# Optimization experiments

Hardware: AMD Instinct MI355X
Metric: run time of the kernel (lower is better)

Reference implementation:

```python
import jax, jax.numpy as jnp
import numpy as np

N_NODES = 150000
D = 64
N_EDGES = 2000000  # bidirectional: 2 * num_train_edges


def setup_inputs() -> dict:
    key = jax.random.key(0)
    k1, k2, k3, k4, k5 = jax.random.split(key, 5)
    nodes_emb = jax.random.normal(k1, (N_NODES, D), dtype=jnp.float32)
    src = jax.random.randint(k2, (N_EDGES,), 0, N_NODES, dtype=jnp.int64 if jax.config.jax_enable_x64 else jnp.int32).astype(jnp.int32)
    dst = jax.random.randint(k3, (N_EDGES,), 0, N_NODES, dtype=jnp.int32)
    W1 = jax.random.normal(k4, (2 * D, D), dtype=jnp.float32) * (1.0 / np.sqrt(2 * D))
    b1 = jnp.zeros((D,), dtype=jnp.float32)
    W2 = jax.random.normal(k5, (D, 1), dtype=jnp.float32) * (1.0 / np.sqrt(D))
    b2 = jnp.zeros((1,), dtype=jnp.float32)
    return {"nodes_emb": nodes_emb, "src": src, "dst": dst,
            "W1": W1, "b1": b1, "W2": W2, "b2": b2}


def reference(nodes_emb, src, dst, W1, b1, W2, b2):
    # Gather per-edge endpoint embeddings and concat: [E, 2D]
    emb_src = nodes_emb[src]          # [E, D]
    emb_dst = nodes_emb[dst]          # [E, D]
    edge_emb = jnp.concatenate([emb_src, emb_dst], axis=1)  # [E, 2D]
    # 2-layer MLP edge scorer: Linear(2D->D) -> ReLU -> Linear(D->1)
    h = jax.nn.relu(edge_emb @ W1 + b1)  # [E, D]
    edge_logits = h @ W2 + b2            # [E, 1]
    return edge_logits
```

## Files before the change

### kernel.cpp

```cpp
#include <hip/hip_runtime.h>

typedef __attribute__((ext_vector_type(8))) short bf16x8;
typedef __attribute__((ext_vector_type(4))) float f32x4;
typedef __attribute__((ext_vector_type(4))) unsigned int u32x4;

#define LDSTR 136
#define TPW 8

static __device__ __forceinline__ unsigned int pack2bf(float x, float y) {
  unsigned int ux = __builtin_bit_cast(unsigned int, x);
  ux += 0x7fffu + ((ux >> 16) & 1u);
  unsigned int uy = __builtin_bit_cast(unsigned int, y);
  uy += 0x7fffu + ((uy >> 16) & 1u);
  return (ux >> 16) | (uy & 0xffff0000u);
}
static __device__ __forceinline__ unsigned short f2bf_s(float x) {
  unsigned int ux = __builtin_bit_cast(unsigned int, x);
  ux += 0x7fffu + ((ux >> 16) & 1u);
  return (unsigned short)(ux >> 16);
}
static __device__ __forceinline__ bf16x8 make_afrag(float4 lo, float4 hi) {
  u32x4 p;
  p[0] = pack2bf(lo.x, lo.y);
  p[1] = pack2bf(lo.z, lo.w);
  p[2] = pack2bf(hi.x, hi.y);
  p[3] = pack2bf(hi.z, hi.w);
  return __builtin_bit_cast(bf16x8, p);
}

__global__ __launch_bounds__(256) void node_proj(
    const float* __restrict__ emb,
    const float* __restrict__ W1,
    unsigned short* __restrict__ P,
    unsigned short* __restrict__ Q,
    int N)
{
  __shared__ unsigned short ls_w1t[64 * LDSTR];
  const int tid  = threadIdx.x;
  const int wave = tid >> 6;
  const int lane = tid & 63;
  const int l15  = lane & 15;
  const int quad = lane >> 4;

  for (int i = tid; i < 64 * 128; i += 256) {
    int n = i >> 7, k = i & 127;
    ls_w1t[n * LDSTR + k] = f2bf_s(W1[k * 64 + n]);
  }
  __syncthreads();

  bf16x8 bfragP[4][2], bfragQ[4][2];
  #pragma unroll
  for (int tn = 0; tn < 4; ++tn)
    #pragma unroll
    for (int s = 0; s < 2; ++s) {
      bfragP[tn][s] = *(const bf16x8*)&ls_w1t[(tn * 16 + l15) * LDSTR + s * 32 + quad * 8];
      bfragQ[tn][s] = *(const bf16x8*)&ls_w1t[(tn * 16 + l15) * LDSTR + 64 + s * 32 + quad * 8];
    }

  const int tile = blockIdx.x * 4 + wave;
  const int base = tile * 16;
  if (base >= N) return;

  bf16x8 afr[2];
  {
    int node = base + l15;
    node = (node < N) ? node : N - 1;
    const float* rp = emb + (long long)node * 64 + quad * 8;
    afr[0] = make_afrag(*(const float4*)(rp),      *(const float4*)(rp + 4));
    afr[1] = make_afrag(*(const float4*)(rp + 32), *(const float4*)(rp + 36));
  }

  f32x4 aP[4], aQ[4];
  #pragma unroll
  for (int tn = 0; tn < 4; ++tn) { aP[tn] = (f32x4){0,0,0,0}; aQ[tn] = (f32x4){0,0,0,0}; }
  #pragma unroll
  for (int s = 0; s < 2; ++s)
    #pragma unroll
    for (int tn = 0; tn < 4; ++tn) {
      aP[tn] = __builtin_amdgcn_mfma_f32_16x16x32_bf16(afr[s], bfragP[tn][s], aP[tn], 0, 0, 0);
      aQ[tn] = __builtin_amdgcn_mfma_f32_16x16x32_bf16(afr[s], bfragQ[tn][s], aQ[tn], 0, 0, 0);
    }

  #pragma unroll
  for (int r = 0; r < 4; ++r) {
    const int m = base + quad * 4 + r;
    if (m < N) {
      #pragma unroll
      for (int tn = 0; tn < 4; ++tn) {
        P[(long long)m * 64 + tn * 16 + l15] = f2bf_s(aP[tn][r]);
        Q[(long long)m * 64 + tn * 16 + l15] = f2bf_s(aQ[tn][r]);
      }
    }
  }
}

__global__ __launch_bounds__(256) void edge_score(
    const unsigned short* __restrict__ P,
    const unsigned short* __restrict__ Q,
    const int*   __restrict__ src,
    const int*   __restrict__ dst,
    const float* __restrict__ b1,
    const float* __restrict__ W2,
    const float* __restrict__ b2,
    float*       __restrict__ out,
    int E)
{
  const int tid  = blockIdx.x * 256 + threadIdx.x;
  const int lane = threadIdx.x & 63;
  const int s    = lane & 7;
  const int g    = lane >> 3;
  const int wid  = tid >> 6;
  const int nwav = gridDim.x * 4;

  float b1v[8], w2v[8];
  {
    const float4 ba = *(const float4*)(b1 + s * 8);
    const float4 bb = *(const float4*)(b1 + s * 8 + 4);
    const float4 wa = *(const float4*)(W2 + s * 8);
    const float4 wb = *(const float4*)(W2 + s * 8 + 4);
    b1v[0]=ba.x; b1v[1]=ba.y; b1v[2]=ba.z; b1v[3]=ba.w;
    b1v[4]=bb.x; b1v[5]=bb.y; b1v[6]=bb.z; b1v[7]=bb.w;
    w2v[0]=wa.x; w2v[1]=wa.y; w2v[2]=wa.z; w2v[3]=wa.w;
    w2v[4]=wb.x; w2v[5]=wb.y; w2v[6]=wb.z; w2v[7]=wb.w;
  }
  const float b2v = b2[0];
  const int so16 = s * 8;

#define DOT8(PV, QV, ACC)                                                     \
  {                                                                           \
    u32x4 pu = __builtin_bit_cast(u32x4, PV);                                 \
    u32x4 qu = __builtin_bit_cast(u32x4, QV);                                 \
    _Pragma("unroll")                                                         \
    for (int i = 0; i < 4; ++i) {                                             \
      float pl = __builtin_bit_cast(float, pu[i] << 16);                      \
      float ph = __builtin_bit_cast(float, pu[i] & 0xffff0000u);              \
      float ql = __builtin_bit_cast(float, qu[i] << 16);                      \
      float qh = __builtin_bit_cast(float, qu[i] & 0xffff0000u);              \
      float h0 = fmaxf(pl + ql + b1v[2 * i], 0.f);                            \
      float h1 = fmaxf(ph + qh + b1v[2 * i + 1], 0.f);                        \
      ACC = __builtin_fmaf(h0, w2v[2 * i], ACC);                              \
      ACC = __builtin_fmaf(h1, w2v[2 * i + 1], ACC);                          \
    }                                                                         \
  }

  const int step = nwav * 16;
  for (int e0 = wid * 16; e0 < E; e0 += step) {
    int eA = e0 + g;
    int eB = e0 + 8 + g;
    const int eAc = (eA < E) ? eA : (E - 1);
    const int eBc = (eB < E) ? eB : (E - 1);
    const int siA = src[eAc], diA = dst[eAc];
    const int siB = src[eBc], diB = dst[eBc];

    const bf16x8 pvA = *(const bf16x8*)(P + (long long)siA * 64 + so16);
    const bf16x8 qvA = *(const bf16x8*)(Q + (long long)diA * 64 + so16);
    const bf16x8 pvB = *(const bf16x8*)(P + (long long)siB * 64 + so16);
    const bf16x8 qvB = *(const bf16x8*)(Q + (long long)diB * 64 + so16);

    float accA = 0.f, accB = 0.f;
    DOT8(pvA, qvA, accA);
    DOT8(pvB, qvB, accB);

    accA += __shfl_xor(accA, 1); accB += __shfl_xor(accB, 1);
    accA += __shfl_xor(accA, 2); accB += __shfl_xor(accB, 2);
    accA += __shfl_xor(accA, 4); accB += __shfl_xor(accB, 4);

    if (s == 0) {
      if (eA < E) out[eA] = accA + b2v;
      if (eB < E) out[eB] = accB + b2v;
    }
  }
#undef DOT8
}

__global__ __launch_bounds__(256) void edge_mlp_f32(
    const float* __restrict__ nodes_emb, const int* __restrict__ src,
    const int* __restrict__ dst, const float* __restrict__ W1,
    const float* __restrict__ b1, const float* __restrict__ W2,
    const float* __restrict__ b2, float* __restrict__ out, int E)
{
  __shared__ unsigned short ls_w1t[64 * LDSTR];
  __shared__ float ls_b1[64];
  __shared__ float ls_w2[64];
  const int tid = threadIdx.x, wave = tid >> 6, lane = tid & 63;
  const int l15 = lane & 15, quad = lane >> 4;
  for (int i = tid; i < 64 * 128; i += 256) {
    int n = i >> 7, k = i & 127;
    ls_w1t[n * LDSTR + k] = f2bf_s(W1[k * 64 + n]);
  }
  if (tid < 64) { ls_b1[tid] = b1[tid]; ls_w2[tid] = W2[tid]; }
  __syncthreads();
  bf16x8 bfrag[4][4];
  #pragma unroll
  for (int tn = 0; tn < 4; ++tn)
    #pragma unroll
    for (int s = 0; s < 4; ++s)
      bfrag[tn][s] = *(const bf16x8*)&ls_w1t[(tn * 16 + l15) * LDSTR + s * 32 + quad * 8];
  float myb1[4], myw2[4];
  #pragma unroll
  for (int tn = 0; tn < 4; ++tn) { myb1[tn] = ls_b1[tn*16+l15]; myw2[tn] = ls_w2[tn*16+l15]; }
  const float b2v = b2[0];
  const int wave_base = blockIdx.x * (TPW * 64) + wave * (TPW * 16);
  #pragma unroll 1
  for (int t = 0; t < TPW; ++t) {
    const int tile_base = wave_base + t * 16;
    if (tile_base >= E) break;
    const int e = tile_base + l15;
    const int si = src[e], di = dst[e];
    const float* srow = nodes_emb + (long long)si * 64 + quad * 8;
    const float* drow = nodes_emb + (long long)di * 64 + quad * 8;
    float4 v0 = *(const float4*)(srow),      v1 = *(const float4*)(srow + 4);
    float4 v2 = *(const float4*)(srow + 32), v3 = *(const float4*)(srow + 36);
    float4 v4 = *(const float4*)(drow),      v5 = *(const float4*)(drow + 4);
    float4 v6 = *(const float4*)(drow + 32), v7 = *(const float4*)(drow + 36);
    bf16x8 afr[4] = {make_afrag(v0,v1), make_afrag(v2,v3), make_afrag(v4,v5), make_afrag(v6,v7)};
    f32x4 acc[4];
    #pragma unroll
    for (int tn = 0; tn < 4; ++tn) acc[tn] = (f32x4){0.f,0.f,0.f,0.f};
    #pragma unroll
    for (int s = 0; s < 4; ++s)
      #pragma unroll
      for (int tn = 0; tn < 4; ++tn)
        acc[tn] = __builtin_amdgcn_mfma_f32_16x16x32_bf16(afr[s], bfrag[tn][s], acc[tn], 0, 0, 0);
    #pragma unroll
    for (int r = 0; r < 4; ++r) {
      float p = 0.f;
      #pragma unroll
      for (int tn = 0; tn < 4; ++tn) {
        float h = fmaxf(acc[tn][r] + myb1[tn], 0.f);
        p = __builtin_fmaf(h, myw2[tn], p);
      }
      p += __shfl_xor(p, 1); p += __shfl_xor(p, 2);
      p += __shfl_xor(p, 4); p += __shfl_xor(p, 8);
      if (l15 == 0) out[tile_base + quad * 4 + r] = p + b2v;
    }
  }
}

extern "C" void kernel_launch(void* const* d_in, const int* in_sizes, int n_in,
                              void* d_out, int out_size, void* d_ws, size_t ws_size,
                              hipStream_t stream) {
  const float* nodes_emb = (const float*)d_in[0];
  const int*   src       = (const int*)d_in[1];
  const int*   dst       = (const int*)d_in[2];
  const float* W1        = (const float*)d_in[3];
  const float* b1        = (const float*)d_in[4];
  const float* W2        = (const float*)d_in[5];
  const float* b2        = (const float*)d_in[6];
  float* out = (float*)d_out;

  const int E = in_sizes[1];
  const int nodes_elems = in_sizes[0];
  const int N = nodes_elems / 64;
  const size_t szP = (size_t)nodes_elems * 2;
  const size_t need = szP * 2;

  if (ws_size >= need) {
    unsigned short* P = (unsigned short*)d_ws;
    unsigned short* Q = (unsigned short*)((char*)d_ws + szP);
    const int ntiles = (N + 15) / 16;
    const int pblocks = (ntiles + 3) / 4;
    hipLaunchKernelGGL(node_proj, dim3(pblocks), dim3(256), 0, stream,
                       nodes_emb, W1, P, Q, N);
    hipLaunchKernelGGL(edge_score, dim3(2048), dim3(256), 0, stream,
                       P, Q, src, dst, b1, W2, b2, out, E);
  } else {
    const int epb = TPW * 64;
    const int blocks = (E + epb - 1) / epb;
    hipLaunchKernelGGL(edge_mlp_f32, dim3(blocks), dim3(256), 0, stream,
                       nodes_emb, src, dst, W1, b1, W2, b2, out, E);
  }
}
```

Before: 203.9 us.

## Permute P/Q channel layout for packed stores and persist node_proj blocks

The node projection now writes P and Q in a permuted channel order, so each lane stores four bf16 values as one 8-byte write instead of four scattered 2-byte writes. The edge scorer remaps b1 and W2 to match this permutation. node_proj becomes a grid-stride loop over 512 persistent blocks, so the W1 transpose and LDS setup are paid once per block instead of once per 4 tiles. The W1 load is also made coalesced. The trade-off is a tighter coupling of layout between the two kernels and fewer blocks in flight.

```diff
diff --git a/kernel.cpp b/kernel.cpp
--- a/kernel.cpp
+++ b/kernel.cpp
@@ -2,6 +2,7 @@
 
 typedef __attribute__((ext_vector_type(8))) short bf16x8;
 typedef __attribute__((ext_vector_type(4))) float f32x4;
+typedef __attribute__((ext_vector_type(2))) unsigned int u32x2;
 typedef __attribute__((ext_vector_type(4))) unsigned int u32x4;
 
 #define LDSTR 136
@@ -31,9 +32,9 @@
 __global__ __launch_bounds__(256) void node_proj(
     const float* __restrict__ emb,
     const float* __restrict__ W1,
-    unsigned short* __restrict__ P,
-    unsigned short* __restrict__ Q,
-    int N)
+    u32x2* __restrict__ P,
+    u32x2* __restrict__ Q,
+    int N, int ntiles)
 {
   __shared__ unsigned short ls_w1t[64 * LDSTR];
   const int tid  = threadIdx.x;
@@ -43,8 +44,8 @@
   const int quad = lane >> 4;
 
   for (int i = tid; i < 64 * 128; i += 256) {
-    int n = i >> 7, k = i & 127;
-    ls_w1t[n * LDSTR + k] = f2bf_s(W1[k * 64 + n]);
+    int k = i >> 6, n = i & 63;
+    ls_w1t[n * LDSTR + k] = f2bf_s(W1[i]);
   }
   __syncthreads();
 
@@ -57,38 +58,40 @@
       bfragQ[tn][s] = *(const bf16x8*)&ls_w1t[(tn * 16 + l15) * LDSTR + 64 + s * 32 + quad * 8];
     }
 
-  const int tile = blockIdx.x * 4 + wave;
-  const int base = tile * 16;
-  if (base >= N) return;
-
-  bf16x8 afr[2];
-  {
-    int node = base + l15;
-    node = (node < N) ? node : N - 1;
-    const float* rp = emb + (long long)node * 64 + quad * 8;
-    afr[0] = make_afrag(*(const float4*)(rp),      *(const float4*)(rp + 4));
-    afr[1] = make_afrag(*(const float4*)(rp + 32), *(const float4*)(rp + 36));
-  }
-
-  f32x4 aP[4], aQ[4];
-  #pragma unroll
-  for (int tn = 0; tn < 4; ++tn) { aP[tn] = (f32x4){0,0,0,0}; aQ[tn] = (f32x4){0,0,0,0}; }
-  #pragma unroll
-  for (int s = 0; s < 2; ++s)
+  for (int tile = blockIdx.x * 4 + wave; tile < ntiles; tile += gridDim.x * 4) {
+    const int base = tile * 16;
+
+    bf16x8 afr0, afr1;
+    {
+      int node = base + l15;
+      node = (node < N) ? node : N - 1;
+      const float* rp = emb + (long long)node * 64 + quad * 8;
+      afr0 = make_afrag(*(const float4*)(rp),      *(const float4*)(rp + 4));
+      afr1 = make_afrag(*(const float4*)(rp + 32), *(const float4*)(rp + 36));
+    }
+
+    f32x4 aP[4], aQ[4];
+    #pragma unroll
+    for (int tn = 0; tn < 4; ++tn) { aP[tn] = (f32x4){0,0,0,0}; aQ[tn] = (f32x4){0,0,0,0}; }
     #pragma unroll
     for (int tn = 0; tn < 4; ++tn) {
-      aP[tn] = __builtin_amdgcn_mfma_f32_16x16x32_bf16(afr[s], bfragP[tn][s], aP[tn], 0, 0, 0);
-      aQ[tn] = __builtin_amdgcn_mfma_f32_16x16x32_bf16(afr[s], bfragQ[tn][s], aQ[tn], 0, 0, 0);
-    }
-
-  #pragma unroll
-  for (int r = 0; r < 4; ++r) {
-    const int m = base + quad * 4 + r;
-    if (m < N) {
-      #pragma unroll
-      for (int tn = 0; tn < 4; ++tn) {
-        P[(long long)m * 64 + tn * 16 + l15] = f2bf_s(aP[tn][r]);
-        Q[(long long)m * 64 + tn * 16 + l15] = f2bf_s(aQ[tn][r]);
+      aP[tn] = __builtin_amdgcn_mfma_f32_16x16x32_bf16(afr0, bfragP[tn][0], aP[tn], 0, 0, 0);
+      aQ[tn] = __builtin_amdgcn_mfma_f32_16x16x32_bf16(afr0, bfragQ[tn][0], aQ[tn], 0, 0, 0);
+      aP[tn] = __builtin_amdgcn_mfma_f32_16x16x32_bf16(afr1, bfragP[tn][1], aP[tn], 0, 0, 0);
+      aQ[tn] = __builtin_amdgcn_mfma_f32_16x16x32_bf16(afr1, bfragQ[tn][1], aQ[tn], 0, 0, 0);
+    }
+
+    #pragma unroll
+    for (int r = 0; r < 4; ++r) {
+      const int m = base + quad * 4 + r;
+      if (m < N) {
+        u32x2 vp, vq;
+        vp[0] = pack2bf(aP[0][r], aP[1][r]);
+        vp[1] = pack2bf(aP[2][r], aP[3][r]);
+        vq[0] = pack2bf(aQ[0][r], aQ[1][r]);
+        vq[1] = pack2bf(aQ[2][r], aQ[3][r]);
+        P[(long long)m * 16 + l15] = vp;
+        Q[(long long)m * 16 + l15] = vq;
       }
     }
   }
@@ -113,15 +116,12 @@
   const int nwav = gridDim.x * 4;
 
   float b1v[8], w2v[8];
-  {
-    const float4 ba = *(const float4*)(b1 + s * 8);
-    const float4 bb = *(const float4*)(b1 + s * 8 + 4);
-    const float4 wa = *(const float4*)(W2 + s * 8);
-    const float4 wb = *(const float4*)(W2 + s * 8 + 4);
-    b1v[0]=ba.x; b1v[1]=ba.y; b1v[2]=ba.z; b1v[3]=ba.w;
-    b1v[4]=bb.x; b1v[5]=bb.y; b1v[6]=bb.z; b1v[7]=bb.w;
-    w2v[0]=wa.x; w2v[1]=wa.y; w2v[2]=wa.z; w2v[3]=wa.w;
-    w2v[4]=wb.x; w2v[5]=wb.y; w2v[6]=wb.z; w2v[7]=wb.w;
+  #pragma unroll
+  for (int j = 0; j < 8; ++j) {
+    const int pos = s * 8 + j;
+    const int ch  = (pos & 3) * 16 + (pos >> 2);
+    b1v[j] = b1[ch];
+    w2v[j] = W2[ch];
   }
   const float b2v = b2[0];
   const int so16 = s * 8;
@@ -256,14 +256,14 @@
   const size_t need = szP * 2;
 
   if (ws_size >= need) {
-    unsigned short* P = (unsigned short*)d_ws;
-    unsigned short* Q = (unsigned short*)((char*)d_ws + szP);
+    u32x2* P = (u32x2*)d_ws;
+    u32x2* Q = (u32x2*)((char*)d_ws + szP);
     const int ntiles = (N + 15) / 16;
-    const int pblocks = (ntiles + 3) / 4;
-    hipLaunchKernelGGL(node_proj, dim3(pblocks), dim3(256), 0, stream,
-                       nodes_emb, W1, P, Q, N);
+    hipLaunchKernelGGL(node_proj, dim3(512), dim3(256), 0, stream,
+                       nodes_emb, W1, P, Q, N, ntiles);
     hipLaunchKernelGGL(edge_score, dim3(2048), dim3(256), 0, stream,
-                       P, Q, src, dst, b1, W2, b2, out, E);
+                       (const unsigned short*)P, (const unsigned short*)Q,
+                       src, dst, b1, W2, b2, out, E);
   } else {
     const int epb = TPW * 64;
     const int blocks = (E + epb - 1) / epb;
```

Result: faster. 173.7 us (-14.8%).
